# Performance work log

Measured on AMD Instinct MI355X. Metric: run time of the kernel, lower is better.

## Reference

```python
import jax, jax.numpy as jnp
import numpy as np

B, T, D, H, L, FF, SPLIT = 2, 4096, 256, 4 * 0 + 8, 4, 1024, 2048
HD = D // H
EPS = 1e-5


def _layernorm(x, s, b):
    mu = jnp.mean(x, axis=-1, keepdims=True)
    var = jnp.mean(jnp.square(x - mu), axis=-1, keepdims=True)
    return (x - mu) * jax.lax.rsqrt(var + EPS) * s + b


def setup_inputs() -> dict:
    key = jax.random.key(0)
    ks = jax.random.split(key, 10)
    sc = 0.02
    inp = {
        "rows": jax.random.normal(ks[0], (B, T, D), jnp.float32),
        "train_target_embeddings": jax.random.normal(ks[1], (B, SPLIT, D), jnp.float32),
        "Wq": sc * jax.random.normal(ks[2], (L, D, D), jnp.float32),
        "bq": jnp.zeros((L, D), jnp.float32),
        "Wk": sc * jax.random.normal(ks[3], (L, D, D), jnp.float32),
        "bk": jnp.zeros((L, D), jnp.float32),
        "Wv": sc * jax.random.normal(ks[4], (L, D, D), jnp.float32),
        "bv": jnp.zeros((L, D), jnp.float32),
        "Wo": sc * jax.random.normal(ks[5], (L, D, D), jnp.float32),
        "bo": jnp.zeros((L, D), jnp.float32),
        "W1": sc * jax.random.normal(ks[6], (L, D, FF), jnp.float32),
        "b1": jnp.zeros((L, FF), jnp.float32),
        "W2": sc * jax.random.normal(ks[7], (L, FF, D), jnp.float32),
        "b2": jnp.zeros((L, D), jnp.float32),
        "ln1_s": jnp.ones((L, D), jnp.float32),
        "ln1_b": jnp.zeros((L, D), jnp.float32),
        "ln2_s": jnp.ones((L, D), jnp.float32),
        "ln2_b": jnp.zeros((L, D), jnp.float32),
        "split": SPLIT,
    }
    return inp


def reference(rows, train_target_embeddings, Wq, bq, Wk, bk, Wv, bv, Wo, bo,
              W1, b1, W2, b2, ln1_s, ln1_b, ln2_s, ln2_b, split):
    # residual add of train target embeddings onto the train rows
    x = rows.at[:, :split, :].add(train_target_embeddings)
    t = x.shape[1]
    # allowed mask: every query can see all train columns; test queries also see themselves
    key_is_train = jnp.arange(t) < split                      # [T]
    allowed = key_is_train[None, :] | jnp.eye(t, dtype=bool)  # [T,T]
    neg = jnp.asarray(-1e9, x.dtype)
    scale = 1.0 / np.sqrt(HD)
    n_layers = Wq.shape[0]
    for l in range(n_layers):
        # multi-head attention with structured mask
        q = (x @ Wq[l] + bq[l]).reshape(x.shape[0], t, H, HD)
        k = (x @ Wk[l] + bk[l]).reshape(x.shape[0], t, H, HD)
        v = (x @ Wv[l] + bv[l]).reshape(x.shape[0], t, H, HD)
        logits = jnp.einsum('bqhd,bkhd->bhqk', q, k) * scale
        logits = jnp.where(allowed[None, None], logits, neg)
        attn = jax.nn.softmax(logits, axis=-1)
        o = jnp.einsum('bhqk,bkhd->bqhd', attn, v).reshape(x.shape[0], t, D)
        x = _layernorm(x + (o @ Wo[l] + bo[l]), ln1_s[l], ln1_b[l])
        # feed-forward
        h = jax.nn.gelu(x @ W1[l] + b1[l])
        x = _layernorm(x + (h @ W2[l] + b2[l]), ln2_s[l], ln2_b[l])
    return x
```

## Files before the change

### kernel.cpp

```cpp
#include <hip/hip_runtime.h>
#include <cstdint>
#include <cstddef>

#define TSEQ 4096
#define BATCH 2
#define DIM 256
#define NHEAD 8
#define HDIM 32
#define NLAYER 4
#define FFDIM 1024
#define SPLITN 2048
#define MROWS (BATCH * TSEQ)

#define QSCALE 0.2550784545f

typedef __attribute__((ext_vector_type(4))) float f32x4;
typedef __attribute__((ext_vector_type(8))) short bf16x8;

__device__ __forceinline__ short f2bf(float f) {
  union { float f; uint32_t u; } v; v.f = f;
  uint32_t r = v.u + 0x7fffu + ((v.u >> 16) & 1u);
  return (short)(r >> 16);
}

__device__ __forceinline__ float bf2f(short s) {
  union { uint32_t u; float f; } v; v.u = ((uint32_t)(uint16_t)s) << 16;
  return v.f;
}

__device__ __forceinline__ float fast_exp2(float x) {
#if __has_builtin(__builtin_amdgcn_exp2f)
  return __builtin_amdgcn_exp2f(x);
#else
  float r;
  asm volatile("v_exp_f32 %0, %1\n\ts_nop 1" : "=v"(r) : "v"(x));
  return r;
#endif
}

__device__ __forceinline__ uint32_t pack2bf(float a, float b) {
  union { float f; uint32_t u; } ua, ub; ua.f = a; ub.f = b;
  return ((ua.u + 0x8000u) >> 16) | ((ub.u + 0x8000u) & 0xffff0000u);
}

__device__ __forceinline__ bf16x8 mk8(uint32_t a, uint32_t b, uint32_t c, uint32_t d) {
  union { uint32_t u[4]; bf16x8 v; } x; x.u[0] = a; x.u[1] = b; x.u[2] = c; x.u[3] = d;
  return x.v;
}

__device__ __forceinline__ float gelu_f(float x) {
  float u = 0.7978845608f * x * (1.0f + 0.044715f * x * x);
  u = fminf(fmaxf(u, -20.f), 20.f);
  float e = fast_exp2(2.885390082f * u);
  float t = (e - 1.0f) / (e + 1.0f);
  return 0.5f * x * (1.0f + t);
}

#define AS1 __attribute__((address_space(1)))
#define AS3 __attribute__((address_space(3)))
__device__ __forceinline__ void gload16(const void* g, void* l) {
  __builtin_amdgcn_global_load_lds((AS1 void*)g, (AS3 void*)l, 16, 0, 0);
}

__global__ __launch_bounds__(256) void prep_w(
    const float* __restrict__ Wq, const float* __restrict__ Wk,
    const float* __restrict__ Wv, const float* __restrict__ Wo,
    const float* __restrict__ W1, const float* __restrict__ W2,
    short* __restrict__ qkvT, short* __restrict__ woT,
    short* __restrict__ w1T, short* __restrict__ w2T)
{
  const int NQKV = NLAYER * 768 * DIM;
  const int NO   = NLAYER * DIM * DIM;
  const int NF   = NLAYER * FFDIM * DIM;
  const int total = NQKV + NO + 2 * NF;
  for (int idx = blockIdx.x * 256 + threadIdx.x; idx < total; idx += gridDim.x * 256) {
    if (idx < NQKV) {
      const int l = idx / (768 * DIM);
      const int rem = idx - l * 768 * DIM;
      const int n = rem >> 8, k = rem & 255;
      const float* src = (n < 256) ? Wq : ((n < 512) ? Wk : Wv);
      qkvT[idx] = f2bf(src[((size_t)l * DIM + k) * DIM + (n & 255)]);
    } else if (idx < NQKV + NO) {
      const int j = idx - NQKV;
      const int l = j >> 16;
      const int rem = j & 65535;
      const int n = rem >> 8, k = rem & 255;
      woT[j] = f2bf(Wo[((size_t)l * DIM + k) * DIM + n]);
    } else if (idx < NQKV + NO + NF) {
      const int j = idx - NQKV - NO;
      const int l = j >> 18;
      const int rem = j & 262143;
      const int n = rem >> 8, k = rem & 255;
      w1T[j] = f2bf(W1[((size_t)l * DIM + k) * FFDIM + n]);
    } else {
      const int j = idx - NQKV - NO - NF;
      const int l = j >> 18;
      const int rem = j & 262143;
      const int n = rem >> 10, k = rem & 1023;
      w2T[j] = f2bf(W2[((size_t)l * FFDIM + k) * DIM + n]);
    }
  }
}

__global__ __launch_bounds__(256) void prep_x(
    const float* __restrict__ rows, const float* __restrict__ tte,
    float* __restrict__ xf, short* __restrict__ xb)
{
  const size_t idx = (size_t)blockIdx.x * 256 + threadIdx.x;
  float4 v = ((const float4*)rows)[idx];
  const size_t e = idx * 4;
  const int m = (int)(e >> 8);
  const int d = (int)(e & 255);
  const int t = m & (TSEQ - 1);
  const int bb = m >> 12;
  if (t < SPLITN) {
    const float4 a = ((const float4*)tte)[((size_t)bb * SPLITN + t) * (DIM / 4) + (d >> 2)];
    v.x += a.x; v.y += a.y; v.z += a.z; v.w += a.w;
  }
  ((float4*)xf)[idx] = v;
  short4 pk; pk.x = f2bf(v.x); pk.y = f2bf(v.y); pk.z = f2bf(v.z); pk.w = f2bf(v.w);
  ((short4*)xb)[idx] = pk;
}

#define GBM 128
#define GBN 64
#define GBK 64

template<int EPI>
__global__ __launch_bounds__(256, 4) void gemm_bt(
    const short* __restrict__ A, const short* __restrict__ BT,
    const float* __restrict__ bias0, const float* __restrict__ bias1,
    const float* __restrict__ bias2, void* __restrict__ Cout,
    int M, int N, int K)
{
  __shared__ short As[GBM * GBK];
  __shared__ short Bs[GBN * GBK];
  const int tid = threadIdx.x;
  const int lane = tid & 63;
  const int wave = tid >> 6;
  const int wm = wave & 1, wn = wave >> 1;
  const int col = lane & 15, quad = lane >> 4;

  const short* Ab = A + (size_t)blockIdx.x * GBM * K;
  const short* Bb = BT + (size_t)blockIdx.y * GBN * K;

  const f32x4 fz = {0.f, 0.f, 0.f, 0.f};
  f32x4 acc[4][2];
#pragma unroll
  for (int i = 0; i < 4; ++i)
#pragma unroll
    for (int j = 0; j < 2; ++j) acc[i][j] = fz;

  for (int k0 = 0; k0 < K; k0 += GBK) {
#pragma unroll
    for (int p = 0; p < 4; ++p) {
      const int i = p * 256 + tid;
      const int r = i >> 3, g = i & 7;
      gload16(Ab + (size_t)r * K + k0 + ((g ^ (r & 7)) * 8), &As[i * 8]);
    }
#pragma unroll
    for (int p = 0; p < 2; ++p) {
      const int i = p * 256 + tid;
      const int r = i >> 3, g = i & 7;
      gload16(Bb + (size_t)r * K + k0 + ((g ^ (r & 7)) * 8), &Bs[i * 8]);
    }
    __syncthreads();
#pragma unroll
    for (int ks = 0; ks < GBK; ks += 32) {
      bf16x8 af[4], bfr[2];
      const int gq = (ks >> 3) + quad;
#pragma unroll
      for (int tm = 0; tm < 4; ++tm) {
        const int row = wm * 64 + tm * 16 + col;
        af[tm] = *(const bf16x8*)&As[row * GBK + ((gq ^ (row & 7)) * 8)];
      }
#pragma unroll
      for (int tn = 0; tn < 2; ++tn) {
        const int row = wn * 32 + tn * 16 + col;
        bfr[tn] = *(const bf16x8*)&Bs[row * GBK + ((gq ^ (row & 7)) * 8)];
      }
#pragma unroll
      for (int tm = 0; tm < 4; ++tm)
#pragma unroll
        for (int tn = 0; tn < 2; ++tn)
          acc[tm][tn] = __builtin_amdgcn_mfma_f32_16x16x32_bf16(af[tm], bfr[tn], acc[tm][tn], 0, 0, 0);
    }
    __syncthreads();
  }

#pragma unroll
  for (int tm = 0; tm < 4; ++tm) {
    const int mbase = blockIdx.x * GBM + wm * 64 + tm * 16 + quad * 4;
#pragma unroll
    for (int tn = 0; tn < 2; ++tn) {
      const int n = blockIdx.y * GBN + wn * 32 + tn * 16 + col;
      float bv;
      if (EPI == 1) bv = (n < 256) ? bias0[n] : ((n < 512) ? bias1[n - 256] : bias2[n - 512]);
      else          bv = bias0[n];
#pragma unroll
      for (int r = 0; r < 4; ++r) {
        float v = acc[tm][tn][r] + bv;
        size_t off = (size_t)(mbase + r) * N + n;
        if (EPI == 1) {
          if (n < 256) v *= QSCALE;
          ((short*)Cout)[off] = f2bf(v);
        } else {
          ((short*)Cout)[off] = f2bf(gelu_f(v));
        }
      }
    }
  }
}

template<int MODE>
__global__ __launch_bounds__(256, 2) void gemm_ln(
    const short* __restrict__ A, const float* __restrict__ Opart,
    const float* __restrict__ lpart,
    const short* __restrict__ BT, const float* __restrict__ bias,
    const float* __restrict__ xres,
    const float* __restrict__ gs, const float* __restrict__ gb,
    float* __restrict__ xoutf, short* __restrict__ xoutb, int K)
{
  __shared__ short As[2][32 * 64];
  __shared__ short Bs[2][256 * 64];
  __shared__ float ssum[4][32], ssq[4][32];
  const int tid = threadIdx.x;
  const int lane = tid & 63;
  const int wave = tid >> 6;
  const int col = lane & 15, quad = lane >> 4;
  const int m0 = blockIdx.x * 32;

  const f32x4 fz = {0.f, 0.f, 0.f, 0.f};
  f32x4 acc[2][4];
#pragma unroll
  for (int i = 0; i < 2; ++i)
#pragma unroll
    for (int j = 0; j < 4; ++j) acc[i][j] = fz;

  const int arow = tid >> 3;
  const int agr  = tid & 7;
  const int grow = m0 + arow;
  const int asw  = (agr ^ (arow & 7)) * 8;

  float4 sa0, sa1, sc0, sc1; float sli = 0.f;

#define STAGE_B(k0_, buf_) do {                                              \
    _Pragma("unroll")                                                        \
    for (int p_ = 0; p_ < 8; ++p_) {                                         \
      const int i_ = p_ * 256 + tid;                                         \
      const int r_ = i_ >> 3, g_ = i_ & 7;                                   \
      gload16(BT + (size_t)r_ * K + (k0_) + ((g_ ^ (r_ & 7)) * 8),           \
              &Bs[buf_][i_ * 8]);                                            \
    } } while (0)

#define STAGE_A_ISSUE(k0_, buf_) do {                                        \
    if (MODE == 0) {                                                         \
      gload16(A + (size_t)grow * K + (k0_) + asw, &As[buf_][tid * 8]);       \
    } else {                                                                 \
      const int tt_ = grow & (TSEQ - 1), bb_ = grow >> 12;                   \
      const int head_ = ((k0_) >> 5) + (agr >= 4 ? 1 : 0);                   \
      const size_t lidx_ = (size_t)(bb_ * 8 + head_) * TSEQ + tt_;           \
      sli = lpart[lidx_] + lpart[(size_t)16 * TSEQ + lidx_];                 \
      const size_t ob_ = (size_t)grow * DIM + (k0_) + agr * 8;               \
      sa0 = *(const float4*)(Opart + ob_);                                   \
      sa1 = *(const float4*)(Opart + ob_ + 4);                               \
      sc0 = *(const float4*)(Opart + (size_t)MROWS * DIM + ob_);             \
      sc1 = *(const float4*)(Opart + (size_t)MROWS * DIM + ob_ + 4);         \
    } } while (0)

#define STAGE_A_WRITE(buf_) do {                                             \
    if (MODE == 1) {                                                         \
      const float li_ = 1.0f / sli;                                          \
      uint4 w_;                                                              \
      w_.x = pack2bf((sa0.x + sc0.x) * li_, (sa0.y + sc0.y) * li_);          \
      w_.y = pack2bf((sa0.z + sc0.z) * li_, (sa0.w + sc0.w) * li_);          \
      w_.z = pack2bf((sa1.x + sc1.x) * li_, (sa1.y + sc1.y) * li_);          \
      w_.w = pack2bf((sa1.z + sc1.z) * li_, (sa1.w + sc1.w) * li_);          \
      *(uint4*)&As[buf_][arow * 64 + asw] = w_;                              \
    } } while (0)

  const int NT = K / 64;
  STAGE_B(0, 0);
  STAGE_A_ISSUE(0, 0);
  STAGE_A_WRITE(0);
  __syncthreads();

  int cur = 0;
  for (int t = 0; t < NT; ++t) {
    if (t + 1 < NT) {
      STAGE_B((t + 1) * 64, cur ^ 1);
      STAGE_A_ISSUE((t + 1) * 64, cur ^ 1);
    }
#pragma unroll
    for (int ks = 0; ks < 64; ks += 32) {
      bf16x8 af[2], bfr[4];
      const int gq = (ks >> 3) + quad;
#pragma unroll
      for (int tm = 0; tm < 2; ++tm) {
        const int row = tm * 16 + col;
        af[tm] = *(const bf16x8*)&As[cur][row * 64 + ((gq ^ (row & 7)) * 8)];
      }
#pragma unroll
      for (int tn = 0; tn < 4; ++tn) {
        const int row = wave * 64 + tn * 16 + col;
        bfr[tn] = *(const bf16x8*)&Bs[cur][row * 64 + ((gq ^ (row & 7)) * 8)];
      }
#pragma unroll
      for (int tm = 0; tm < 2; ++tm)
#pragma unroll
        for (int tn = 0; tn < 4; ++tn)
          acc[tm][tn] = __builtin_amdgcn_mfma_f32_16x16x32_bf16(af[tm], bfr[tn], acc[tm][tn], 0, 0, 0);
    }
    if (t + 1 < NT) STAGE_A_WRITE(cur ^ 1);
    __syncthreads();
    cur ^= 1;
  }
#undef STAGE_B
#undef STAGE_A_ISSUE
#undef STAGE_A_WRITE

  const float* resb = xres + (size_t)m0 * DIM;
#pragma unroll
  for (int tn = 0; tn < 4; ++tn) {
    const int n = wave * 64 + tn * 16 + col;
    const float bv = bias[n];
#pragma unroll
    for (int tm = 0; tm < 2; ++tm)
#pragma unroll
      for (int r = 0; r < 4; ++r) {
        const int row = tm * 16 + quad * 4 + r;
        acc[tm][tn][r] += bv + resb[(size_t)row * DIM + n];
      }
  }

#pragma unroll
  for (int tm = 0; tm < 2; ++tm)
#pragma unroll
    for (int r = 0; r < 4; ++r) {
      float s = 0.f, q = 0.f;
#pragma unroll
      for (int tn = 0; tn < 4; ++tn) { const float v = acc[tm][tn][r]; s += v; q += v * v; }
      s += __shfl_xor(s, 1); q += __shfl_xor(q, 1);
      s += __shfl_xor(s, 2); q += __shfl_xor(q, 2);
      s += __shfl_xor(s, 4); q += __shfl_xor(q, 4);
      s += __shfl_xor(s, 8); q += __shfl_xor(q, 8);
      if (col == 0) { const int row = tm * 16 + quad * 4 + r; ssum[wave][row] = s; ssq[wave][row] = q; }
    }
  __syncthreads();
  if (tid < 32) {
    const float S = ssum[0][tid] + ssum[1][tid] + ssum[2][tid] + ssum[3][tid];
    const float Q = ssq[0][tid] + ssq[1][tid] + ssq[2][tid] + ssq[3][tid];
    const float mu = S * (1.0f / DIM);
    const float var = Q * (1.0f / DIM) - mu * mu;
    ssum[0][tid] = mu;
    ssq[0][tid] = rsqrtf(var + 1e-5f);
  }
  __syncthreads();

#pragma unroll
  for (int tm = 0; tm < 2; ++tm)
#pragma unroll
    for (int tn = 0; tn < 4; ++tn) {
      const int n = wave * 64 + tn * 16 + col;
      const float g = gs[n], bb = gb[n];
#pragma unroll
      for (int r = 0; r < 4; ++r) {
        const int row = tm * 16 + quad * 4 + r;
        const float out = (acc[tm][tn][r] - ssum[0][row]) * ssq[0][row] * g + bb;
        xoutf[(size_t)(m0 + row) * DIM + n] = out;
        xoutb[(size_t)(m0 + row) * DIM + n] = f2bf(out);
      }
    }
}

#define AKT 64
#define KSPL 1024
#define NKT (KSPL / AKT)

__global__ __launch_bounds__(256, 4) void attn_kernel(
    const short* __restrict__ qkv,
    float* __restrict__ Opart, float* __restrict__ lpart)
{
  __shared__ short Kbuf[2][AKT * HDIM];
  __shared__ short Vbuf[2][HDIM * AKT];
  __shared__ float Pdiag[4][16];

  const int tid = threadIdx.x;
  const int lane = tid & 63;
  const int wave = tid >> 6;
  const int col = lane & 15, quad = lane >> 4;
  const int bh = blockIdx.y;
  const int b = bh >> 3, h = bh & 7;
  const int hz = blockIdx.z;
  const int q0 = blockIdx.x * 128 + wave * 32;

  const short* qbase = qkv + (size_t)b * TSEQ * 768 + h * HDIM;
  const short* kbase = qbase + 256;
  const short* vcol  = qbase + 512;

  const short* ksrc = kbase + (size_t)(hz * KSPL + (tid & 63)) * 768 + (tid >> 6) * 8;
  const int vkey = tid & 63, vhg = tid >> 6;
  const int vs = vkey >> 4, vqd = (vkey >> 2) & 3, vrr = vkey & 3;
  const int vpos = (vs >> 1) * 32 + vqd * 8 + (vs & 1) * 4 + vrr;
  const int vgs = vpos >> 3, vo8 = vpos & 7;
  const short* vsrc = vcol + (size_t)(hz * KSPL + vkey) * 768 + vhg * 8;

  const bf16x8 qf0 = *(const bf16x8*)(qbase + (size_t)(q0 + col) * 768 + quad * 8);
  const bf16x8 qf1 = *(const bf16x8*)(qbase + (size_t)(q0 + 16 + col) * 768 + quad * 8);

  bf16x8 ones;
#pragma unroll
  for (int i = 0; i < 8; ++i) ones[i] = (short)0x3F80;

  const f32x4 fz = {0.f, 0.f, 0.f, 0.f};
  f32x4 o[2][2] = {{fz, fz}, {fz, fz}};
  f32x4 lacc[2] = {fz, fz};

  gload16(ksrc, &Kbuf[0][tid * 8]);
  {
    const bf16x8 v0 = *(const bf16x8*)vsrc;
#pragma unroll
    for (int j = 0; j < 8; ++j)
      Vbuf[0][(vhg * 8 + j) * 64 + ((vgs ^ j) * 8) + vo8] = v0[j];
  }
  bf16x8 vnext = *(const bf16x8*)(vsrc + (size_t)AKT * 768);

  int cur = 0;
  for (int t = 0; t < NKT; ++t) {
    __syncthreads();
    if (t + 1 < NKT) {
      gload16(ksrc + (size_t)(t + 1) * AKT * 768, &Kbuf[1 - cur][tid * 8]);
#pragma unroll
      for (int j = 0; j < 8; ++j)
        Vbuf[1 - cur][(vhg * 8 + j) * 64 + ((vgs ^ j) * 8) + vo8] = vnext[j];
      if (t + 2 < NKT) vnext = *(const bf16x8*)(vsrc + (size_t)(t + 2) * AKT * 768);
    }
    const short* kb = Kbuf[cur];
    const short* vb = Vbuf[cur];

    uint32_t pw0[8], pw1[8];
#pragma unroll
    for (int st = 0; st < 4; ++st) {
      const bf16x8 kf = *(const bf16x8*)&kb[(quad * 64 + st * 16 + col) * 8];
      const f32x4 s0 = __builtin_amdgcn_mfma_f32_16x16x32_bf16(kf, qf0, fz, 0, 0, 0);
      const f32x4 s1 = __builtin_amdgcn_mfma_f32_16x16x32_bf16(kf, qf1, fz, 0, 0, 0);
      pw0[st * 2]     = pack2bf(fast_exp2(s0[0]), fast_exp2(s0[1]));
      pw0[st * 2 + 1] = pack2bf(fast_exp2(s0[2]), fast_exp2(s0[3]));
      pw1[st * 2]     = pack2bf(fast_exp2(s1[0]), fast_exp2(s1[1]));
      pw1[st * 2 + 1] = pack2bf(fast_exp2(s1[2]), fast_exp2(s1[3]));
    }

#pragma unroll
    for (int kh = 0; kh < 2; ++kh) {
      const bf16x8 pf0 = mk8(pw0[kh * 4], pw0[kh * 4 + 1], pw0[kh * 4 + 2], pw0[kh * 4 + 3]);
      const bf16x8 pf1 = mk8(pw1[kh * 4], pw1[kh * 4 + 1], pw1[kh * 4 + 2], pw1[kh * 4 + 3]);
#pragma unroll
      for (int hh = 0; hh < 2; ++hh) {
        const int hd = hh * 16 + col;
        const bf16x8 vf = *(const bf16x8*)&vb[hd * AKT + (((kh * 4 + quad) ^ (hd & 7)) * 8)];
        o[0][hh] = __builtin_amdgcn_mfma_f32_16x16x32_bf16(pf0, vf, o[0][hh], 0, 0, 0);
        o[1][hh] = __builtin_amdgcn_mfma_f32_16x16x32_bf16(pf1, vf, o[1][hh], 0, 0, 0);
      }
      lacc[0] = __builtin_amdgcn_mfma_f32_16x16x32_bf16(pf0, ones, lacc[0], 0, 0, 0);
      lacc[1] = __builtin_amdgcn_mfma_f32_16x16x32_bf16(pf1, ones, lacc[1], 0, 0, 0);
    }
    cur ^= 1;
  }

  if (hz == 1 && blockIdx.x >= SPLITN / 128) {
#pragma unroll
    for (int qsub = 0; qsub < 2; ++qsub) {
      const int qd = q0 + qsub * 16;
      const bf16x8 qf = qsub ? qf1 : qf0;
      const bf16x8 kf = *(const bf16x8*)(kbase + (size_t)(qd + col) * 768 + quad * 8);
      const f32x4 sd = __builtin_amdgcn_mfma_f32_16x16x32_bf16(kf, qf, fz, 0, 0, 0);
      float ps = 0.f;
#pragma unroll
      for (int r = 0; r < 4; ++r)
        if (quad * 4 + r == col) ps = fast_exp2(sd[r]);
      if (quad == (col >> 2)) Pdiag[wave][col] = ps;
      asm volatile("s_waitcnt lgkmcnt(0)" ::: "memory");
      const f32x4 pv = *(const f32x4*)&Pdiag[wave][quad * 4];
#pragma unroll
      for (int r = 0; r < 4; ++r) {
        lacc[qsub][r] += pv[r];
        const size_t vrow = (size_t)(qd + quad * 4 + r) * 768;
#pragma unroll
        for (int hh = 0; hh < 2; ++hh)
          o[qsub][hh][r] += pv[r] * bf2f(vcol[vrow + hh * 16 + col]);
      }
      asm volatile("s_waitcnt lgkmcnt(0)" ::: "memory");
    }
  }

  float* Ob = Opart + (size_t)hz * MROWS * DIM;
  float* lb = lpart + (size_t)hz * 16 * TSEQ + (size_t)bh * TSEQ;
#pragma unroll
  for (int qsub = 0; qsub < 2; ++qsub) {
    const f32x4 la = lacc[qsub];
    const int qq = q0 + qsub * 16 + quad * 4;
    const int rowb = b * TSEQ + qq;
#pragma unroll
    for (int r = 0; r < 4; ++r) {
      if (col == 0) lb[qq + r] = la[r];
#pragma unroll
      for (int hh = 0; hh < 2; ++hh)
        Ob[(size_t)(rowb + r) * DIM + h * HDIM + hh * 16 + col] = o[qsub][hh][r];
    }
  }
}

extern "C" void kernel_launch(void* const* d_in, const int* in_sizes, int n_in,
                              void* d_out, int out_size, void* d_ws, size_t ws_size,
                              hipStream_t stream)
{
  const float* rows = (const float*)d_in[0];
  const float* tte  = (const float*)d_in[1];
  const float* Wq = (const float*)d_in[2];  const float* bq = (const float*)d_in[3];
  const float* Wk = (const float*)d_in[4];  const float* bk = (const float*)d_in[5];
  const float* Wv = (const float*)d_in[6];  const float* bv = (const float*)d_in[7];
  const float* Wo = (const float*)d_in[8];  const float* bo = (const float*)d_in[9];
  const float* W1 = (const float*)d_in[10]; const float* b1 = (const float*)d_in[11];
  const float* W2 = (const float*)d_in[12]; const float* b2 = (const float*)d_in[13];
  const float* ln1s = (const float*)d_in[14]; const float* ln1b = (const float*)d_in[15];
  const float* ln2s = (const float*)d_in[16]; const float* ln2b = (const float*)d_in[17];

  char* p = (char*)d_ws;
  float* xf   = (float*)p;  p += (size_t)MROWS * DIM * 4;
  short* xb   = (short*)p;  p += (size_t)MROWS * DIM * 2;
  short* qkv  = (short*)p;  p += (size_t)MROWS * 768 * 2;
  short* hb   = (short*)p;  p += (size_t)MROWS * FFDIM * 2;
  float* Opart = (float*)p; p += (size_t)2 * MROWS * DIM * 4;
  float* lpart = (float*)p; p += (size_t)2 * 16 * TSEQ * 4;
  short* qkvT = (short*)p;  p += (size_t)NLAYER * 768 * DIM * 2;
  short* woT  = (short*)p;  p += (size_t)NLAYER * DIM * DIM * 2;
  short* w1T  = (short*)p;  p += (size_t)NLAYER * FFDIM * DIM * 2;
  short* w2T  = (short*)p;  p += (size_t)NLAYER * DIM * FFDIM * 2;

  prep_w<<<2048, 256, 0, stream>>>(Wq, Wk, Wv, Wo, W1, W2, qkvT, woT, w1T, w2T);
  prep_x<<<MROWS * DIM / 4 / 256, 256, 0, stream>>>(rows, tte, xf, xb);

  for (int l = 0; l < NLAYER; ++l) {
    gemm_bt<1><<<dim3(MROWS / GBM, 768 / GBN), 256, 0, stream>>>(
        xb, qkvT + (size_t)l * 768 * DIM, bq + l * DIM, bk + l * DIM, bv + l * DIM,
        qkv, MROWS, 768, DIM);
    attn_kernel<<<dim3(TSEQ / 128, BATCH * NHEAD, 2), 256, 0, stream>>>(qkv, Opart, lpart);
    gemm_ln<1><<<MROWS / 32, 256, 0, stream>>>(
        nullptr, Opart, lpart, woT + (size_t)l * DIM * DIM, bo + l * DIM, xf,
        ln1s + l * DIM, ln1b + l * DIM, xf, xb, DIM);
    gemm_bt<3><<<dim3(MROWS / GBM, FFDIM / GBN), 256, 0, stream>>>(
        xb, w1T + (size_t)l * FFDIM * DIM, b1 + l * FFDIM, nullptr, nullptr,
        hb, MROWS, FFDIM, DIM);
    float* xo = (l == NLAYER - 1) ? (float*)d_out : xf;
    gemm_ln<0><<<MROWS / 32, 256, 0, stream>>>(
        hb, nullptr, nullptr, w2T + (size_t)l * DIM * FFDIM,
        b2 + l * DIM, xf, ln2s + l * DIM, ln2b + l * DIM, xo, xb, FFDIM);
  }
}
```

Baseline: 488.0 us.

## Drop attention key split; normalize in-kernel and emit bf16 output directly

The attention kernel no longer splits the 2048 train keys across two z-blocks writing fp32 partial outputs and row sums. Each block now covers 64 queries, with each wave handling 16 queries over all keys in 128-key tiles, and it divides by the row sum before writing bf16 output. The output-projection GEMM+LayerNorm then reads that bf16 buffer directly, removing the template mode that summed the partials and converted them. This cuts fp32 partial traffic and the conversion work, but halves per-wave query reuse of K/V tiles and reduces parallelism within each block.

```diff
diff --git a/kernel.cpp b/kernel.cpp
--- a/kernel.cpp
+++ b/kernel.cpp
@@ -212,10 +212,8 @@
   }
 }
 
-template<int MODE>
 __global__ __launch_bounds__(256, 2) void gemm_ln(
-    const short* __restrict__ A, const float* __restrict__ Opart,
-    const float* __restrict__ lpart,
+    const short* __restrict__ A,
     const short* __restrict__ BT, const float* __restrict__ bias,
     const float* __restrict__ xres,
     const float* __restrict__ gs, const float* __restrict__ gb,
@@ -242,8 +240,6 @@
   const int grow = m0 + arow;
   const int asw  = (agr ^ (arow & 7)) * 8;
 
-  float4 sa0, sa1, sc0, sc1; float sli = 0.f;
-
 #define STAGE_B(k0_, buf_) do {                                              \
     _Pragma("unroll")                                                        \
     for (int p_ = 0; p_ < 8; ++p_) {                                         \
@@ -253,43 +249,19 @@
               &Bs[buf_][i_ * 8]);                                            \
     } } while (0)
 
-#define STAGE_A_ISSUE(k0_, buf_) do {                                        \
-    if (MODE == 0) {                                                         \
-      gload16(A + (size_t)grow * K + (k0_) + asw, &As[buf_][tid * 8]);       \
-    } else {                                                                 \
-      const int tt_ = grow & (TSEQ - 1), bb_ = grow >> 12;                   \
-      const int head_ = ((k0_) >> 5) + (agr >= 4 ? 1 : 0);                   \
-      const size_t lidx_ = (size_t)(bb_ * 8 + head_) * TSEQ + tt_;           \
-      sli = lpart[lidx_] + lpart[(size_t)16 * TSEQ + lidx_];                 \
-      const size_t ob_ = (size_t)grow * DIM + (k0_) + agr * 8;               \
-      sa0 = *(const float4*)(Opart + ob_);                                   \
-      sa1 = *(const float4*)(Opart + ob_ + 4);                               \
-      sc0 = *(const float4*)(Opart + (size_t)MROWS * DIM + ob_);             \
-      sc1 = *(const float4*)(Opart + (size_t)MROWS * DIM + ob_ + 4);         \
-    } } while (0)
-
-#define STAGE_A_WRITE(buf_) do {                                             \
-    if (MODE == 1) {                                                         \
-      const float li_ = 1.0f / sli;                                          \
-      uint4 w_;                                                              \
-      w_.x = pack2bf((sa0.x + sc0.x) * li_, (sa0.y + sc0.y) * li_);          \
-      w_.y = pack2bf((sa0.z + sc0.z) * li_, (sa0.w + sc0.w) * li_);          \
-      w_.z = pack2bf((sa1.x + sc1.x) * li_, (sa1.y + sc1.y) * li_);          \
-      w_.w = pack2bf((sa1.z + sc1.z) * li_, (sa1.w + sc1.w) * li_);          \
-      *(uint4*)&As[buf_][arow * 64 + asw] = w_;                              \
-    } } while (0)
+#define STAGE_A(k0_, buf_)                                                   \
+    gload16(A + (size_t)grow * K + (k0_) + asw, &As[buf_][tid * 8])
 
   const int NT = K / 64;
   STAGE_B(0, 0);
-  STAGE_A_ISSUE(0, 0);
-  STAGE_A_WRITE(0);
+  STAGE_A(0, 0);
   __syncthreads();
 
   int cur = 0;
   for (int t = 0; t < NT; ++t) {
     if (t + 1 < NT) {
       STAGE_B((t + 1) * 64, cur ^ 1);
-      STAGE_A_ISSUE((t + 1) * 64, cur ^ 1);
+      STAGE_A((t + 1) * 64, cur ^ 1);
     }
 #pragma unroll
     for (int ks = 0; ks < 64; ks += 32) {
@@ -311,13 +283,11 @@
         for (int tn = 0; tn < 4; ++tn)
           acc[tm][tn] = __builtin_amdgcn_mfma_f32_16x16x32_bf16(af[tm], bfr[tn], acc[tm][tn], 0, 0, 0);
     }
-    if (t + 1 < NT) STAGE_A_WRITE(cur ^ 1);
     __syncthreads();
     cur ^= 1;
   }
 #undef STAGE_B
-#undef STAGE_A_ISSUE
-#undef STAGE_A_WRITE
+#undef STAGE_A
 
   const float* resb = xres + (size_t)m0 * DIM;
 #pragma unroll
@@ -373,15 +343,13 @@
     }
 }
 
-#define AKT 64
-#define KSPL 1024
-#define NKT (KSPL / AKT)
+#define AKT 128
+#define NKT (SPLITN / AKT)
 
 __global__ __launch_bounds__(256, 4) void attn_kernel(
-    const short* __restrict__ qkv,
-    float* __restrict__ Opart, float* __restrict__ lpart)
+    const short* __restrict__ qkv, short* __restrict__ ob)
 {
-  __shared__ short Kbuf[2][AKT * HDIM];
+  __shared__ short Kbuf[2][4 * AKT * 8];
   __shared__ short Vbuf[2][HDIM * AKT];
   __shared__ float Pdiag[4][16];
 
@@ -391,122 +359,119 @@
   const int col = lane & 15, quad = lane >> 4;
   const int bh = blockIdx.y;
   const int b = bh >> 3, h = bh & 7;
-  const int hz = blockIdx.z;
-  const int q0 = blockIdx.x * 128 + wave * 32;
+  const int q0 = blockIdx.x * 64 + wave * 16;
 
   const short* qbase = qkv + (size_t)b * TSEQ * 768 + h * HDIM;
   const short* kbase = qbase + 256;
   const short* vcol  = qbase + 512;
 
-  const short* ksrc = kbase + (size_t)(hz * KSPL + (tid & 63)) * 768 + (tid >> 6) * 8;
+  const short* ksrc = kbase + (size_t)(tid & 63) * 768 + (tid >> 6) * 8;
   const int vkey = tid & 63, vhg = tid >> 6;
-  const int vs = vkey >> 4, vqd = (vkey >> 2) & 3, vrr = vkey & 3;
-  const int vpos = (vs >> 1) * 32 + vqd * 8 + (vs & 1) * 4 + vrr;
-  const int vgs = vpos >> 3, vo8 = vpos & 7;
-  const short* vsrc = vcol + (size_t)(hz * KSPL + vkey) * 768 + vhg * 8;
-
-  const bf16x8 qf0 = *(const bf16x8*)(qbase + (size_t)(q0 + col) * 768 + quad * 8);
-  const bf16x8 qf1 = *(const bf16x8*)(qbase + (size_t)(q0 + 16 + col) * 768 + quad * 8);
+  int vgs[2], vo8[2];
+#pragma unroll
+  for (int p = 0; p < 2; ++p) {
+    const int kk = p * 64 + vkey;
+    const int vs = kk >> 4, vqd = (kk >> 2) & 3, vrr = kk & 3;
+    const int vpos = (vs >> 1) * 32 + vqd * 8 + (vs & 1) * 4 + vrr;
+    vgs[p] = vpos >> 3; vo8[p] = vpos & 7;
+  }
+  const short* vsrc0 = vcol + (size_t)vkey * 768 + vhg * 8;
+  const short* vsrc1 = vsrc0 + (size_t)64 * 768;
+
+  const bf16x8 qf = *(const bf16x8*)(qbase + (size_t)(q0 + col) * 768 + quad * 8);
 
   bf16x8 ones;
 #pragma unroll
   for (int i = 0; i < 8; ++i) ones[i] = (short)0x3F80;
 
   const f32x4 fz = {0.f, 0.f, 0.f, 0.f};
-  f32x4 o[2][2] = {{fz, fz}, {fz, fz}};
-  f32x4 lacc[2] = {fz, fz};
-
-  gload16(ksrc, &Kbuf[0][tid * 8]);
+  f32x4 o[2] = {fz, fz};
+  f32x4 lacc = fz;
+
+  gload16(ksrc, &Kbuf[0][wave * 1024 + lane * 8]);
+  gload16(ksrc + (size_t)64 * 768, &Kbuf[0][wave * 1024 + 512 + lane * 8]);
   {
-    const bf16x8 v0 = *(const bf16x8*)vsrc;
-#pragma unroll
-    for (int j = 0; j < 8; ++j)
-      Vbuf[0][(vhg * 8 + j) * 64 + ((vgs ^ j) * 8) + vo8] = v0[j];
-  }
-  bf16x8 vnext = *(const bf16x8*)(vsrc + (size_t)AKT * 768);
+    const bf16x8 v0 = *(const bf16x8*)vsrc0;
+    const bf16x8 v1 = *(const bf16x8*)vsrc1;
+#pragma unroll
+    for (int j = 0; j < 8; ++j) {
+      Vbuf[0][(vhg * 8 + j) * AKT + ((vgs[0] ^ j) * 8) + vo8[0]] = v0[j];
+      Vbuf[0][(vhg * 8 + j) * AKT + ((vgs[1] ^ j) * 8) + vo8[1]] = v1[j];
+    }
+  }
+  bf16x8 vna = *(const bf16x8*)(vsrc0 + (size_t)AKT * 768);
+  bf16x8 vnb = *(const bf16x8*)(vsrc1 + (size_t)AKT * 768);
 
   int cur = 0;
   for (int t = 0; t < NKT; ++t) {
     __syncthreads();
     if (t + 1 < NKT) {
-      gload16(ksrc + (size_t)(t + 1) * AKT * 768, &Kbuf[1 - cur][tid * 8]);
-#pragma unroll
-      for (int j = 0; j < 8; ++j)
-        Vbuf[1 - cur][(vhg * 8 + j) * 64 + ((vgs ^ j) * 8) + vo8] = vnext[j];
-      if (t + 2 < NKT) vnext = *(const bf16x8*)(vsrc + (size_t)(t + 2) * AKT * 768);
+      const size_t koff = (size_t)(t + 1) * AKT * 768;
+      gload16(ksrc + koff, &Kbuf[1 - cur][wave * 1024 + lane * 8]);
+      gload16(ksrc + koff + (size_t)64 * 768, &Kbuf[1 - cur][wave * 1024 + 512 + lane * 8]);
+#pragma unroll
+      for (int j = 0; j < 8; ++j) {
+        Vbuf[1 - cur][(vhg * 8 + j) * AKT + ((vgs[0] ^ j) * 8) + vo8[0]] = vna[j];
+        Vbuf[1 - cur][(vhg * 8 + j) * AKT + ((vgs[1] ^ j) * 8) + vo8[1]] = vnb[j];
+      }
+      if (t + 2 < NKT) {
+        vna = *(const bf16x8*)(vsrc0 + (size_t)(t + 2) * AKT * 768);
+        vnb = *(const bf16x8*)(vsrc1 + (size_t)(t + 2) * AKT * 768);
+      }
     }
     const short* kb = Kbuf[cur];
     const short* vb = Vbuf[cur];
 
-    uint32_t pw0[8], pw1[8];
-#pragma unroll
-    for (int st = 0; st < 4; ++st) {
-      const bf16x8 kf = *(const bf16x8*)&kb[(quad * 64 + st * 16 + col) * 8];
-      const f32x4 s0 = __builtin_amdgcn_mfma_f32_16x16x32_bf16(kf, qf0, fz, 0, 0, 0);
-      const f32x4 s1 = __builtin_amdgcn_mfma_f32_16x16x32_bf16(kf, qf1, fz, 0, 0, 0);
-      pw0[st * 2]     = pack2bf(fast_exp2(s0[0]), fast_exp2(s0[1]));
-      pw0[st * 2 + 1] = pack2bf(fast_exp2(s0[2]), fast_exp2(s0[3]));
-      pw1[st * 2]     = pack2bf(fast_exp2(s1[0]), fast_exp2(s1[1]));
-      pw1[st * 2 + 1] = pack2bf(fast_exp2(s1[2]), fast_exp2(s1[3]));
-    }
-
-#pragma unroll
-    for (int kh = 0; kh < 2; ++kh) {
-      const bf16x8 pf0 = mk8(pw0[kh * 4], pw0[kh * 4 + 1], pw0[kh * 4 + 2], pw0[kh * 4 + 3]);
-      const bf16x8 pf1 = mk8(pw1[kh * 4], pw1[kh * 4 + 1], pw1[kh * 4 + 2], pw1[kh * 4 + 3]);
+    uint32_t pw[16];
+#pragma unroll
+    for (int st = 0; st < 8; ++st) {
+      const bf16x8 kf = *(const bf16x8*)&kb[quad * 1024 + (st * 16 + col) * 8];
+      const f32x4 s = __builtin_amdgcn_mfma_f32_16x16x32_bf16(kf, qf, fz, 0, 0, 0);
+      pw[st * 2]     = pack2bf(fast_exp2(s[0]), fast_exp2(s[1]));
+      pw[st * 2 + 1] = pack2bf(fast_exp2(s[2]), fast_exp2(s[3]));
+    }
+
+#pragma unroll
+    for (int kh = 0; kh < 4; ++kh) {
+      const bf16x8 pf = mk8(pw[kh * 4], pw[kh * 4 + 1], pw[kh * 4 + 2], pw[kh * 4 + 3]);
 #pragma unroll
       for (int hh = 0; hh < 2; ++hh) {
         const int hd = hh * 16 + col;
         const bf16x8 vf = *(const bf16x8*)&vb[hd * AKT + (((kh * 4 + quad) ^ (hd & 7)) * 8)];
-        o[0][hh] = __builtin_amdgcn_mfma_f32_16x16x32_bf16(pf0, vf, o[0][hh], 0, 0, 0);
-        o[1][hh] = __builtin_amdgcn_mfma_f32_16x16x32_bf16(pf1, vf, o[1][hh], 0, 0, 0);
-      }
-      lacc[0] = __builtin_amdgcn_mfma_f32_16x16x32_bf16(pf0, ones, lacc[0], 0, 0, 0);
-      lacc[1] = __builtin_amdgcn_mfma_f32_16x16x32_bf16(pf1, ones, lacc[1], 0, 0, 0);
+        o[hh] = __builtin_amdgcn_mfma_f32_16x16x32_bf16(pf, vf, o[hh], 0, 0, 0);
+      }
+      lacc = __builtin_amdgcn_mfma_f32_16x16x32_bf16(pf, ones, lacc, 0, 0, 0);
     }
     cur ^= 1;
   }
 
-  if (hz == 1 && blockIdx.x >= SPLITN / 128) {
-#pragma unroll
-    for (int qsub = 0; qsub < 2; ++qsub) {
-      const int qd = q0 + qsub * 16;
-      const bf16x8 qf = qsub ? qf1 : qf0;
-      const bf16x8 kf = *(const bf16x8*)(kbase + (size_t)(qd + col) * 768 + quad * 8);
-      const f32x4 sd = __builtin_amdgcn_mfma_f32_16x16x32_bf16(kf, qf, fz, 0, 0, 0);
-      float ps = 0.f;
-#pragma unroll
-      for (int r = 0; r < 4; ++r)
-        if (quad * 4 + r == col) ps = fast_exp2(sd[r]);
-      if (quad == (col >> 2)) Pdiag[wave][col] = ps;
-      asm volatile("s_waitcnt lgkmcnt(0)" ::: "memory");
-      const f32x4 pv = *(const f32x4*)&Pdiag[wave][quad * 4];
-#pragma unroll
-      for (int r = 0; r < 4; ++r) {
-        lacc[qsub][r] += pv[r];
-        const size_t vrow = (size_t)(qd + quad * 4 + r) * 768;
-#pragma unroll
-        for (int hh = 0; hh < 2; ++hh)
-          o[qsub][hh][r] += pv[r] * bf2f(vcol[vrow + hh * 16 + col]);
-      }
-      asm volatile("s_waitcnt lgkmcnt(0)" ::: "memory");
-    }
-  }
-
-  float* Ob = Opart + (size_t)hz * MROWS * DIM;
-  float* lb = lpart + (size_t)hz * 16 * TSEQ + (size_t)bh * TSEQ;
-#pragma unroll
-  for (int qsub = 0; qsub < 2; ++qsub) {
-    const f32x4 la = lacc[qsub];
-    const int qq = q0 + qsub * 16 + quad * 4;
-    const int rowb = b * TSEQ + qq;
+  if (q0 >= SPLITN) {
+    const bf16x8 kfd = *(const bf16x8*)(kbase + (size_t)(q0 + col) * 768 + quad * 8);
+    const f32x4 sd = __builtin_amdgcn_mfma_f32_16x16x32_bf16(kfd, qf, fz, 0, 0, 0);
+    float ps = 0.f;
+#pragma unroll
+    for (int r = 0; r < 4; ++r)
+      if (quad * 4 + r == col) ps = fast_exp2(sd[r]);
+    if (quad == (col >> 2)) Pdiag[wave][col] = ps;
+    asm volatile("s_waitcnt lgkmcnt(0)" ::: "memory");
+    const f32x4 pv = *(const f32x4*)&Pdiag[wave][quad * 4];
 #pragma unroll
     for (int r = 0; r < 4; ++r) {
-      if (col == 0) lb[qq + r] = la[r];
+      lacc[r] += pv[r];
+      const size_t vrow = (size_t)(q0 + quad * 4 + r) * 768;
 #pragma unroll
       for (int hh = 0; hh < 2; ++hh)
-        Ob[(size_t)(rowb + r) * DIM + h * HDIM + hh * 16 + col] = o[qsub][hh][r];
-    }
+        o[hh][r] += pv[r] * bf2f(vcol[vrow + hh * 16 + col]);
+    }
+  }
+
+#pragma unroll
+  for (int r = 0; r < 4; ++r) {
+    const float inv = 1.0f / lacc[r];
+    const size_t row = (size_t)b * TSEQ + q0 + quad * 4 + r;
+#pragma unroll
+    for (int hh = 0; hh < 2; ++hh)
+      ob[row * DIM + h * HDIM + hh * 16 + col] = f2bf(o[hh][r] * inv);
   }
 }
 
@@ -530,8 +495,7 @@
   short* xb   = (short*)p;  p += (size_t)MROWS * DIM * 2;
   short* qkv  = (short*)p;  p += (size_t)MROWS * 768 * 2;
   short* hb   = (short*)p;  p += (size_t)MROWS * FFDIM * 2;
-  float* Opart = (float*)p; p += (size_t)2 * MROWS * DIM * 4;
-  float* lpart = (float*)p; p += (size_t)2 * 16 * TSEQ * 4;
+  short* ob   = (short*)p;  p += (size_t)MROWS * DIM * 2;
   short* qkvT = (short*)p;  p += (size_t)NLAYER * 768 * DIM * 2;
   short* woT  = (short*)p;  p += (size_t)NLAYER * DIM * DIM * 2;
   short* w1T  = (short*)p;  p += (size_t)NLAYER * FFDIM * DIM * 2;
@@ -544,16 +508,16 @@
     gemm_bt<1><<<dim3(MROWS / GBM, 768 / GBN), 256, 0, stream>>>(
         xb, qkvT + (size_t)l * 768 * DIM, bq + l * DIM, bk + l * DIM, bv + l * DIM,
         qkv, MROWS, 768, DIM);
-    attn_kernel<<<dim3(TSEQ / 128, BATCH * NHEAD, 2), 256, 0, stream>>>(qkv, Opart, lpart);
-    gemm_ln<1><<<MROWS / 32, 256, 0, stream>>>(
-        nullptr, Opart, lpart, woT + (size_t)l * DIM * DIM, bo + l * DIM, xf,
+    attn_kernel<<<dim3(TSEQ / 64, BATCH * NHEAD), 256, 0, stream>>>(qkv, ob);
+    gemm_ln<<<MROWS / 32, 256, 0, stream>>>(
+        ob, woT + (size_t)l * DIM * DIM, bo + l * DIM, xf,
         ln1s + l * DIM, ln1b + l * DIM, xf, xb, DIM);
     gemm_bt<3><<<dim3(MROWS / GBM, FFDIM / GBN), 256, 0, stream>>>(
         xb, w1T + (size_t)l * FFDIM * DIM, b1 + l * FFDIM, nullptr, nullptr,
         hb, MROWS, FFDIM, DIM);
     float* xo = (l == NLAYER - 1) ? (float*)d_out : xf;
-    gemm_ln<0><<<MROWS / 32, 256, 0, stream>>>(
-        hb, nullptr, nullptr, w2T + (size_t)l * DIM * FFDIM,
+    gemm_ln<<<MROWS / 32, 256, 0, stream>>>(
+        hb, w2T + (size_t)l * DIM * FFDIM,
         b2 + l * DIM, xf, ln2s + l * DIM, ln2b + l * DIM, xo, xb, FFDIM);
   }
 }
```

Measured after the change: 558.6 us. 14.5% more time.

## Remove attention key-split and normalize attention output in-kernel as bf16

Applied to the files above, without the earlier changes.

Attention blocks now iterate over all train keys instead of splitting them across two grid slices. The kernel normalizes by the softmax row sum itself and writes a bf16 output. This removes the fp32 partial-output and row-sum buffers and their combine step in the Wo GEMM, cutting global memory traffic. The cost is half as many attention blocks, so there is less parallelism and less latency hiding on a large GPU.

```diff
diff --git a/kernel.cpp b/kernel.cpp
--- a/kernel.cpp
+++ b/kernel.cpp
@@ -212,10 +212,8 @@
   }
 }
 
-template<int MODE>
 __global__ __launch_bounds__(256, 2) void gemm_ln(
-    const short* __restrict__ A, const float* __restrict__ Opart,
-    const float* __restrict__ lpart,
+    const short* __restrict__ A,
     const short* __restrict__ BT, const float* __restrict__ bias,
     const float* __restrict__ xres,
     const float* __restrict__ gs, const float* __restrict__ gb,
@@ -242,8 +240,6 @@
   const int grow = m0 + arow;
   const int asw  = (agr ^ (arow & 7)) * 8;
 
-  float4 sa0, sa1, sc0, sc1; float sli = 0.f;
-
 #define STAGE_B(k0_, buf_) do {                                              \
     _Pragma("unroll")                                                        \
     for (int p_ = 0; p_ < 8; ++p_) {                                         \
@@ -253,43 +249,19 @@
               &Bs[buf_][i_ * 8]);                                            \
     } } while (0)
 
-#define STAGE_A_ISSUE(k0_, buf_) do {                                        \
-    if (MODE == 0) {                                                         \
-      gload16(A + (size_t)grow * K + (k0_) + asw, &As[buf_][tid * 8]);       \
-    } else {                                                                 \
-      const int tt_ = grow & (TSEQ - 1), bb_ = grow >> 12;                   \
-      const int head_ = ((k0_) >> 5) + (agr >= 4 ? 1 : 0);                   \
-      const size_t lidx_ = (size_t)(bb_ * 8 + head_) * TSEQ + tt_;           \
-      sli = lpart[lidx_] + lpart[(size_t)16 * TSEQ + lidx_];                 \
-      const size_t ob_ = (size_t)grow * DIM + (k0_) + agr * 8;               \
-      sa0 = *(const float4*)(Opart + ob_);                                   \
-      sa1 = *(const float4*)(Opart + ob_ + 4);                               \
-      sc0 = *(const float4*)(Opart + (size_t)MROWS * DIM + ob_);             \
-      sc1 = *(const float4*)(Opart + (size_t)MROWS * DIM + ob_ + 4);         \
-    } } while (0)
-
-#define STAGE_A_WRITE(buf_) do {                                             \
-    if (MODE == 1) {                                                         \
-      const float li_ = 1.0f / sli;                                          \
-      uint4 w_;                                                              \
-      w_.x = pack2bf((sa0.x + sc0.x) * li_, (sa0.y + sc0.y) * li_);          \
-      w_.y = pack2bf((sa0.z + sc0.z) * li_, (sa0.w + sc0.w) * li_);          \
-      w_.z = pack2bf((sa1.x + sc1.x) * li_, (sa1.y + sc1.y) * li_);          \
-      w_.w = pack2bf((sa1.z + sc1.z) * li_, (sa1.w + sc1.w) * li_);          \
-      *(uint4*)&As[buf_][arow * 64 + asw] = w_;                              \
-    } } while (0)
+#define STAGE_A(k0_, buf_)                                                   \
+    gload16(A + (size_t)grow * K + (k0_) + asw, &As[buf_][tid * 8])
 
   const int NT = K / 64;
   STAGE_B(0, 0);
-  STAGE_A_ISSUE(0, 0);
-  STAGE_A_WRITE(0);
+  STAGE_A(0, 0);
   __syncthreads();
 
   int cur = 0;
   for (int t = 0; t < NT; ++t) {
     if (t + 1 < NT) {
       STAGE_B((t + 1) * 64, cur ^ 1);
-      STAGE_A_ISSUE((t + 1) * 64, cur ^ 1);
+      STAGE_A((t + 1) * 64, cur ^ 1);
     }
 #pragma unroll
     for (int ks = 0; ks < 64; ks += 32) {
@@ -311,13 +283,11 @@
         for (int tn = 0; tn < 4; ++tn)
           acc[tm][tn] = __builtin_amdgcn_mfma_f32_16x16x32_bf16(af[tm], bfr[tn], acc[tm][tn], 0, 0, 0);
     }
-    if (t + 1 < NT) STAGE_A_WRITE(cur ^ 1);
     __syncthreads();
     cur ^= 1;
   }
 #undef STAGE_B
-#undef STAGE_A_ISSUE
-#undef STAGE_A_WRITE
+#undef STAGE_A
 
   const float* resb = xres + (size_t)m0 * DIM;
 #pragma unroll
@@ -374,12 +344,10 @@
 }
 
 #define AKT 64
-#define KSPL 1024
-#define NKT (KSPL / AKT)
+#define NKT (SPLITN / AKT)
 
 __global__ __launch_bounds__(256, 4) void attn_kernel(
-    const short* __restrict__ qkv,
-    float* __restrict__ Opart, float* __restrict__ lpart)
+    const short* __restrict__ qkv, short* __restrict__ ob)
 {
   __shared__ short Kbuf[2][AKT * HDIM];
   __shared__ short Vbuf[2][HDIM * AKT];
@@ -391,19 +359,18 @@
   const int col = lane & 15, quad = lane >> 4;
   const int bh = blockIdx.y;
   const int b = bh >> 3, h = bh & 7;
-  const int hz = blockIdx.z;
   const int q0 = blockIdx.x * 128 + wave * 32;
 
   const short* qbase = qkv + (size_t)b * TSEQ * 768 + h * HDIM;
   const short* kbase = qbase + 256;
   const short* vcol  = qbase + 512;
 
-  const short* ksrc = kbase + (size_t)(hz * KSPL + (tid & 63)) * 768 + (tid >> 6) * 8;
+  const short* ksrc = kbase + (size_t)(tid & 63) * 768 + (tid >> 6) * 8;
   const int vkey = tid & 63, vhg = tid >> 6;
   const int vs = vkey >> 4, vqd = (vkey >> 2) & 3, vrr = vkey & 3;
   const int vpos = (vs >> 1) * 32 + vqd * 8 + (vs & 1) * 4 + vrr;
   const int vgs = vpos >> 3, vo8 = vpos & 7;
-  const short* vsrc = vcol + (size_t)(hz * KSPL + vkey) * 768 + vhg * 8;
+  const short* vsrc = vcol + (size_t)vkey * 768 + vhg * 8;
 
   const bf16x8 qf0 = *(const bf16x8*)(qbase + (size_t)(q0 + col) * 768 + quad * 8);
   const bf16x8 qf1 = *(const bf16x8*)(qbase + (size_t)(q0 + 16 + col) * 768 + quad * 8);
@@ -467,7 +434,7 @@
     cur ^= 1;
   }
 
-  if (hz == 1 && blockIdx.x >= SPLITN / 128) {
+  if (blockIdx.x >= SPLITN / 128) {
 #pragma unroll
     for (int qsub = 0; qsub < 2; ++qsub) {
       const int qd = q0 + qsub * 16;
@@ -493,19 +460,15 @@
     }
   }
 
-  float* Ob = Opart + (size_t)hz * MROWS * DIM;
-  float* lb = lpart + (size_t)hz * 16 * TSEQ + (size_t)bh * TSEQ;
 #pragma unroll
   for (int qsub = 0; qsub < 2; ++qsub) {
-    const f32x4 la = lacc[qsub];
-    const int qq = q0 + qsub * 16 + quad * 4;
-    const int rowb = b * TSEQ + qq;
 #pragma unroll
     for (int r = 0; r < 4; ++r) {
-      if (col == 0) lb[qq + r] = la[r];
+      const float inv = 1.0f / lacc[qsub][r];
+      const size_t row = (size_t)b * TSEQ + q0 + qsub * 16 + quad * 4 + r;
 #pragma unroll
       for (int hh = 0; hh < 2; ++hh)
-        Ob[(size_t)(rowb + r) * DIM + h * HDIM + hh * 16 + col] = o[qsub][hh][r];
+        ob[row * DIM + h * HDIM + hh * 16 + col] = f2bf(o[qsub][hh][r] * inv);
     }
   }
 }
@@ -530,8 +493,7 @@
   short* xb   = (short*)p;  p += (size_t)MROWS * DIM * 2;
   short* qkv  = (short*)p;  p += (size_t)MROWS * 768 * 2;
   short* hb   = (short*)p;  p += (size_t)MROWS * FFDIM * 2;
-  float* Opart = (float*)p; p += (size_t)2 * MROWS * DIM * 4;
-  float* lpart = (float*)p; p += (size_t)2 * 16 * TSEQ * 4;
+  short* ob   = (short*)p;  p += (size_t)MROWS * DIM * 2;
   short* qkvT = (short*)p;  p += (size_t)NLAYER * 768 * DIM * 2;
   short* woT  = (short*)p;  p += (size_t)NLAYER * DIM * DIM * 2;
   short* w1T  = (short*)p;  p += (size_t)NLAYER * FFDIM * DIM * 2;
@@ -544,16 +506,16 @@
     gemm_bt<1><<<dim3(MROWS / GBM, 768 / GBN), 256, 0, stream>>>(
         xb, qkvT + (size_t)l * 768 * DIM, bq + l * DIM, bk + l * DIM, bv + l * DIM,
         qkv, MROWS, 768, DIM);
-    attn_kernel<<<dim3(TSEQ / 128, BATCH * NHEAD, 2), 256, 0, stream>>>(qkv, Opart, lpart);
-    gemm_ln<1><<<MROWS / 32, 256, 0, stream>>>(
-        nullptr, Opart, lpart, woT + (size_t)l * DIM * DIM, bo + l * DIM, xf,
+    attn_kernel<<<dim3(TSEQ / 128, BATCH * NHEAD), 256, 0, stream>>>(qkv, ob);
+    gemm_ln<<<MROWS / 32, 256, 0, stream>>>(
+        ob, woT + (size_t)l * DIM * DIM, bo + l * DIM, xf,
         ln1s + l * DIM, ln1b + l * DIM, xf, xb, DIM);
     gemm_bt<3><<<dim3(MROWS / GBM, FFDIM / GBN), 256, 0, stream>>>(
         xb, w1T + (size_t)l * FFDIM * DIM, b1 + l * FFDIM, nullptr, nullptr,
         hb, MROWS, FFDIM, DIM);
     float* xo = (l == NLAYER - 1) ? (float*)d_out : xf;
-    gemm_ln<0><<<MROWS / 32, 256, 0, stream>>>(
-        hb, nullptr, nullptr, w2T + (size_t)l * DIM * FFDIM,
+    gemm_ln<<<MROWS / 32, 256, 0, stream>>>(
+        hb, w2T + (size_t)l * DIM * FFDIM,
         b2 + l * DIM, xf, ln2s + l * DIM, ln2b + l * DIM, xo, xb, FFDIM);
   }
 }
```

After: 479.6 us. No clear change (-1.7%).
